# Performance work log

Hardware: AMD Instinct MI355X
Metric: run time of the kernel (lower is better)

## Reference

```python
import jax, jax.numpy as jnp
import numpy as np

I3 = jnp.eye(3, dtype=jnp.float32)
G_VEC = jnp.array([0.0, 0.0, -9.80665], dtype=jnp.float32)
# Q diag: [cov_omega x3, cov_acc x3, cov_b_omega x3, cov_b_acc x3, cov_Rot_c_i x3, cov_t_c_i x3]
Q_DIAG = jnp.array([1e-3] * 3 + [1e-2] * 3 + [6e-9] * 3 + [2e-4] * 3 + [1e-9] * 3 + [1e-9] * 3, dtype=jnp.float32)
N_NORM_ROT = 100
N_NORM_ROT_CI = 1000


def skew(v):
    z = jnp.zeros_like(v[0])
    return jnp.stack([jnp.stack([z, -v[2], v[1]]),
                      jnp.stack([v[2], z, -v[0]]),
                      jnp.stack([-v[1], v[0], z])])


def so3exp(phi):
    a2 = jnp.sum(phi * phi)
    small = a2 < 1e-12
    a = jnp.sqrt(jnp.where(small, 1.0, a2))
    axis = phi / a
    c, s = jnp.cos(a), jnp.sin(a)
    big = c * I3 + (1.0 - c) * jnp.outer(axis, axis) + s * skew(axis)
    return jnp.where(small, I3 + skew(phi), big)


def sen3exp(xi):
    # SE_2(3) exponential: xi[:3]=rotation, xi[3:9]=(v, p) parts
    phi = xi[:3]
    a2 = jnp.sum(phi * phi)
    small = a2 < 1e-12
    a = jnp.sqrt(jnp.where(small, 1.0, a2))
    axis = phi / a
    c, s = jnp.cos(a), jnp.sin(a)
    sk = skew(axis)
    R = jnp.where(small, I3 + skew(phi),
                  c * I3 + (1.0 - c) * jnp.outer(axis, axis) + s * sk)
    J = jnp.where(small, I3 + 0.5 * skew(phi),
                  (s / a) * I3 + (1.0 - s / a) * jnp.outer(axis, axis) + ((1.0 - c) / a) * sk)
    x = J @ xi[3:].reshape(2, 3).T  # (3,2): columns are dv, dp
    return R, x


def normalize_rot(R):
    # Polar-factor re-orthonormalization (equivalent to the SVD-based
    # normalize_rot for near-rotation matrices), via Newton-Schulz iteration
    # which is smooth and jit/vjp friendly.
    def body(X, _):
        return 1.5 * X - 0.5 * (X @ X.T @ X), None
    X, _ = jax.lax.scan(body, R, None, length=8)
    return X


def from_rpy(roll, pitch, yaw):
    cr, sr = jnp.cos(roll), jnp.sin(roll)
    cp, sp = jnp.cos(pitch), jnp.sin(pitch)
    cy, sy = jnp.cos(yaw), jnp.sin(yaw)
    one = jnp.ones_like(cr)
    zero = jnp.zeros_like(cr)
    Rx = jnp.stack([jnp.stack([one, zero, zero]), jnp.stack([zero, cr, -sr]), jnp.stack([zero, sr, cr])])
    Ry = jnp.stack([jnp.stack([cp, zero, sp]), jnp.stack([zero, one, zero]), jnp.stack([-sp, zero, cp])])
    Rz = jnp.stack([jnp.stack([cy, -sy, zero]), jnp.stack([sy, cy, zero]), jnp.stack([zero, zero, one])])
    return Rz @ Ry @ Rx


def init_covariance():
    P = jnp.zeros((21, 21), dtype=jnp.float32)
    P = P.at[:2, :2].set(1e-3 * jnp.eye(2))     # cov_Rot0 (no yaw error)
    P = P.at[3:5, 3:5].set(0.1 * jnp.eye(2))    # cov_v0
    P = P.at[9:12, 9:12].set(6e-3 * I3)         # cov_b_omega0
    P = P.at[12:15, 12:15].set(4e-3 * I3)       # cov_b_acc0
    P = P.at[15:18, 15:18].set(1e-6 * I3)       # cov_Rot_c_i0
    P = P.at[18:21, 18:21].set(5e-3 * I3)       # cov_t_c_i0
    return P


def propagate_cov(P, Rot, v, p, dt):
    F = jnp.zeros((21, 21), dtype=P.dtype)
    F = F.at[3:6, :3].set(skew(G_VEC))
    F = F.at[6:9, 3:6].set(I3)
    F = F.at[:3, 9:12].set(-Rot)
    F = F.at[3:6, 9:12].set(-skew(v) @ Rot)
    F = F.at[3:6, 12:15].set(-Rot)
    F = F.at[6:9, 9:12].set(-skew(p) @ Rot)
    G = jnp.zeros((21, 18), dtype=P.dtype)
    G = G.at[:3, :3].set(Rot)
    G = G.at[3:6, 3:6].set(Rot)
    G = G.at[9:12, 6:9].set(I3)
    G = G.at[12:15, 9:12].set(I3)
    G = G.at[15:18, 12:15].set(I3)
    G = G.at[18:21, 15:18].set(I3)
    F = F * dt
    G = G * dt
    F2 = F @ F
    Phi = jnp.eye(21, dtype=P.dtype) + F + 0.5 * F2 + (F2 @ F) / 6.0  # 3rd-order expm
    return Phi @ (P + (G * Q_DIAG[None, :]) @ G.T) @ Phi.T


def _step(carry, xs):
    Rot, v, p, b_om, b_ac, Rci, tci, P = carry
    u_i, dt_i, mcov_i, i = xs
    # ---- propagate ----
    acc = Rot @ (u_i[3:6] - b_ac) + G_VEC
    v_n = v + acc * dt_i
    p_n = p + v * dt_i + 0.5 * acc * dt_i * dt_i
    Rot_n = Rot @ so3exp((u_i[:3] - b_om) * dt_i)
    P_n = propagate_cov(P, Rot, v, p, dt_i)
    # ---- update: zero lateral/vertical body-velocity pseudo-measurement ----
    omega = u_i[:3] - b_om
    Rot_body = Rot_n @ Rci
    v_imu = Rot_n.T @ v_n
    v_body = Rci.T @ v_imu + skew(tci) @ omega
    H = jnp.zeros((2, 21), dtype=P.dtype)
    H = H.at[:, 3:6].set(Rot_body.T[1:])
    H = H.at[:, 15:18].set((Rci.T @ skew(v_imu))[1:])
    H = H.at[:, 9:12].set(skew(tci)[1:])
    H = H.at[:, 18:21].set(-skew(omega)[1:])
    r = -v_body[1:]
    Rm = jnp.diag(mcov_i)
    S = H @ P_n @ H.T + Rm                    # (2,2)
    K = jnp.linalg.solve(S, H @ P_n).T        # K = P H^T S^-1 (P, S symmetric)
    dx = K @ r                                 # (21,)
    dR, dxi = sen3exp(dx[:9])
    Rot_u = dR @ Rot_n
    v_u = dR @ v_n + dxi[:, 0]
    p_u = dR @ p_n + dxi[:, 1]
    b_om_u = b_om + dx[9:12]
    b_ac_u = b_ac + dx[12:15]
    Rci_u = so3exp(dx[15:18]) @ Rci
    tci_u = tci + dx[18:21]
    IKH = jnp.eye(21, dtype=P.dtype) - K @ H
    P_u = IKH @ P_n @ IKH.T + K @ Rm @ K.T    # Joseph form
    P_u = 0.5 * (P_u + P_u.T)
    Rot_u = jnp.where(i % N_NORM_ROT == 0, normalize_rot(Rot_u), Rot_u)
    Rci_u = jnp.where(i % N_NORM_ROT_CI == 0, normalize_rot(Rci_u), Rci_u)
    carry = (Rot_u, v_u, p_u, b_om_u, b_ac_u, Rci_u, tci_u, P_u)
    return carry, (Rot_u, v_u, p_u, b_om_u, b_ac_u, Rci_u, tci_u)


def _forward(t, u, measurements_covs, v_mes, p_mes, ang0, N):
    dt = t[1:N] - t[:N - 1]
    Rot0 = from_rpy(ang0[0], ang0[1], ang0[2])
    z3 = jnp.zeros(3, dtype=u.dtype)
    carry0 = (Rot0, v_mes[0], z3, z3, z3, I3, z3, init_covariance())
    xs = (u[1:N], dt, measurements_covs[1:N], jnp.arange(1, N))
    _, ys = jax.lax.scan(_step, carry0, xs)
    Rot = jnp.concatenate([Rot0[None], ys[0]], axis=0)
    v = jnp.concatenate([v_mes[0][None], ys[1]], axis=0)
    p = jnp.concatenate([z3[None], ys[2]], axis=0)
    b_omega = jnp.concatenate([z3[None], ys[3]], axis=0)
    b_acc = jnp.concatenate([z3[None], ys[4]], axis=0)
    Rot_c_i = jnp.concatenate([I3[None], ys[5]], axis=0)
    t_c_i = jnp.concatenate([z3[None], ys[6]], axis=0)
    return (Rot, v, p, b_omega, b_acc, Rot_c_i, t_c_i)


def setup_inputs() -> dict:
    key = jax.random.key(0)
    N = 20000  # 200 s at 100 Hz IMU
    k0, k1, k2, k3, k4, k5 = jax.random.split(key, 6)
    t = jnp.arange(N, dtype=jnp.float32) * 0.01
    gyro = 0.01 * jax.random.normal(k0, (N, 3), dtype=jnp.float32)
    acc = jnp.array([0.0, 0.0, 9.80665], jnp.float32) + 0.1 * jax.random.normal(k1, (N, 3), dtype=jnp.float32)
    u = jnp.concatenate([gyro, acc], axis=1)
    measurements_covs = 0.1 + jax.random.uniform(k2, (N, 2), dtype=jnp.float32)
    v_mes = jax.random.normal(k3, (N, 3), dtype=jnp.float32)
    p_mes = jax.random.normal(k4, (N, 3), dtype=jnp.float32)
    ang0 = 0.01 * jax.random.normal(k5, (3,), dtype=jnp.float32)
    return dict(t=t, u=u, measurements_covs=measurements_covs, v_mes=v_mes, p_mes=p_mes, ang0=ang0, N=N)


def reference(t, u, measurements_covs, v_mes, p_mes, ang0, N):
    return _forward(t, u, measurements_covs, v_mes, p_mes, ang0, N)
```

## Files before the change

### kernel.cpp

```cpp
#include <hip/hip_runtime.h>

#define GRAV 9.80665f
#define WAVE_SYNC() do { \
    asm volatile("s_waitcnt lgkmcnt(0)" ::: "memory"); \
    __builtin_amdgcn_sched_barrier(0); \
  } while(0)

#define LDP 28

__device__ __forceinline__ float sel3(int r, float a0, float a1, float a2){
  float x = (r==1)? a1 : a0;
  return (r>=2)? a2 : x;
}
__device__ __forceinline__ float RL(float v, int k){
  return __int_as_float(__builtin_amdgcn_readlane(__float_as_int(v), k));
}
__device__ __forceinline__ float pick9(int k, const float* X){
  float s=X[0];
  s=(k==1)?X[1]:s; s=(k==2)?X[2]:s; s=(k==3)?X[3]:s; s=(k==4)?X[4]:s;
  s=(k==5)?X[5]:s; s=(k==6)?X[6]:s; s=(k==7)?X[7]:s; s=(k==8)?X[8]:s;
  return s;
}

__device__ __forceinline__ void mm33(float* __restrict__ O, const float* A, const float* B){
#pragma unroll
  for(int r=0;r<3;++r){
#pragma unroll
    for(int c=0;c<3;++c){
      O[r*3+c] = A[r*3+0]*B[0*3+c] + A[r*3+1]*B[1*3+c] + A[r*3+2]*B[2*3+c];
    }
  }
}

__device__ __forceinline__ void rot_from_t2(float t_, float p0, float p1, float p2, float* R){
  float c_, k1_, k2_;
  if (t_ < 1e-4f){
    c_  = 1.f - t_*(0.5f - t_*((1.f/24.f) - t_*(1.f/720.f)));
    k2_ = 1.f - t_*((1.f/6.f) - t_*((1.f/120.f) - t_*(1.f/5040.f)));
    k1_ = 0.5f - t_*((1.f/24.f) - t_*(1.f/720.f));
  } else {
    float a = sqrtf(t_);
    c_ = __cosf(a);
    float s = __sinf(a);
    k2_ = s/a;
    k1_ = (1.f - c_)/t_;
  }
  R[0]=c_+k1_*p0*p0;      R[1]=k1_*p0*p1-k2_*p2;  R[2]=k1_*p0*p2+k2_*p1;
  R[3]=k1_*p0*p1+k2_*p2;  R[4]=c_+k1_*p1*p1;      R[5]=k1_*p1*p2-k2_*p0;
  R[6]=k1_*p0*p2-k2_*p1;  R[7]=k1_*p1*p2+k2_*p0;  R[8]=c_+k1_*p2*p2;
}

__device__ __forceinline__ void normalize_rot9(float* X){
#pragma unroll 1
  for(int it=0; it<8; ++it){
    float Y[9], Z[9];
#pragma unroll
    for(int r=0;r<3;++r)
#pragma unroll
      for(int c=0;c<3;++c)
        Y[r*3+c] = X[r*3+0]*X[c*3+0] + X[r*3+1]*X[c*3+1] + X[r*3+2]*X[c*3+2];
#pragma unroll
    for(int r=0;r<3;++r)
#pragma unroll
      for(int c=0;c<3;++c)
        Z[r*3+c] = Y[r*3+0]*X[0*3+c] + Y[r*3+1]*X[1*3+c] + Y[r*3+2]*X[2*3+c];
#pragma unroll
    for(int e=0;e<9;++e) X[e] = 1.5f*X[e] - 0.5f*Z[e];
  }
}

__device__ __forceinline__ float pick_state(int l,
    const float* Rt, const float* vv, const float* pp,
    const float* bw, const float* ba, const float* Rc, const float* tc){
  float s = Rt[0];
  s=(l==1)?Rt[1]:s;  s=(l==2)?Rt[2]:s;  s=(l==3)?Rt[3]:s;  s=(l==4)?Rt[4]:s;
  s=(l==5)?Rt[5]:s;  s=(l==6)?Rt[6]:s;  s=(l==7)?Rt[7]:s;  s=(l==8)?Rt[8]:s;
  s=(l==9)?vv[0]:s;  s=(l==10)?vv[1]:s; s=(l==11)?vv[2]:s;
  s=(l==12)?pp[0]:s; s=(l==13)?pp[1]:s; s=(l==14)?pp[2]:s;
  s=(l==15)?bw[0]:s; s=(l==16)?bw[1]:s; s=(l==17)?bw[2]:s;
  s=(l==18)?ba[0]:s; s=(l==19)?ba[1]:s; s=(l==20)?ba[2]:s;
  s=(l==21)?Rc[0]:s; s=(l==22)?Rc[1]:s; s=(l==23)?Rc[2]:s;
  s=(l==24)?Rc[3]:s; s=(l==25)?Rc[4]:s; s=(l==26)?Rc[5]:s;
  s=(l==27)?Rc[6]:s; s=(l==28)?Rc[7]:s; s=(l==29)?Rc[8]:s;
  s=(l==30)?tc[0]:s; s=(l==31)?tc[1]:s; s=(l==32)?tc[2]:s;
  return s;
}

__global__ __launch_bounds__(64,1)
void iekf_scan_kernel(const float* __restrict__ t,
                      const float* __restrict__ u,
                      const float* __restrict__ mcov,
                      const float* __restrict__ v_mes,
                      const float* __restrict__ ang0,
                      float* __restrict__ out, int N)
{
  const int l = threadIdx.x;
  __shared__ __align__(16) float Pm[21*LDP];
  __shared__ __align__(16) float Eb[21*LDP];

  for (int e=l; e<21*LDP; e+=64){
    int r=e/LDP, c=e-(e/LDP)*LDP;
    float vI=0.f;
    if (r==c){
      if (r<2) vI=0.001f;
      else if (r==3||r==4) vI=0.1f;
      else if (r>=9&&r<12) vI=0.006f;
      else if (r>=12&&r<15) vI=0.004f;
      else if (r>=15&&r<18) vI=1e-6f;
      else if (r>=18&&r<21) vI=0.005f;
    }
    Pm[e]=vI;
  }

  int ostr=0; float* op = out;
  {
    int obase=0, ooff=0;
    if (l<9)       {obase=0;    ostr=9; ooff=l;}
    else if (l<12) {obase=9*N;  ostr=3; ooff=l-9;}
    else if (l<15) {obase=12*N; ostr=3; ooff=l-12;}
    else if (l<18) {obase=15*N; ostr=3; ooff=l-15;}
    else if (l<21) {obase=18*N; ostr=3; ooff=l-18;}
    else if (l<30) {obase=21*N; ostr=9; ooff=l-21;}
    else           {obase=30*N; ostr=3; ooff=l-30;}
    op = out + obase + ooff;
  }

  const int g21 = l/21;
  const int c21 = l - g21*21;
  const int cw  = 9 + 4*g21;
  int l1 = l+21; if (l1>=63) l1-=63;
  int l2 = l+42; if (l2>=63) l2-=63;
  static const int cols[12] = {3,4,5, 9,10,11, 15,16,17, 18,19,20};

  float myval = 0.f;
  {
    float Rt0[9], vv0[3], pp0[3], bwa[3], baa[3], Rc0[9], tca[3];
    float rl = ang0[0], pt = ang0[1], yw = ang0[2];
    float cr=cosf(rl), sr=sinf(rl), cp=cosf(pt), sp=sinf(pt), cy=cosf(yw), sy=sinf(yw);
    Rt0[0]=cy*cp; Rt0[1]=cy*sp*sr - sy*cr; Rt0[2]=cy*sp*cr + sy*sr;
    Rt0[3]=sy*cp; Rt0[4]=sy*sp*sr + cy*cr; Rt0[5]=sy*sp*cr - cy*sr;
    Rt0[6]=-sp;   Rt0[7]=cp*sr;            Rt0[8]=cp*cr;
    vv0[0]=v_mes[0]; vv0[1]=v_mes[1]; vv0[2]=v_mes[2];
#pragma unroll
    for(int k=0;k<3;++k){ pp0[k]=0.f; bwa[k]=0.f; baa[k]=0.f; tca[k]=0.f; }
    Rc0[0]=1.f;Rc0[1]=0.f;Rc0[2]=0.f;Rc0[3]=0.f;Rc0[4]=1.f;Rc0[5]=0.f;Rc0[6]=0.f;Rc0[7]=0.f;Rc0[8]=1.f;
    float sv = pick_state(l, Rt0, vv0, pp0, bwa, baa, Rc0, tca);
    if (l<33){ op[0] = sv; myval = sv; }
  }
  WAVE_SYNC();

  float tA = t[0], tB = t[1];
  float cu[6];
#pragma unroll
  for(int k=0;k<6;++k) cu[k]=u[6+k];
  float cm0=mcov[2], cm1=mcov[3];

  int nx100=100, nx1000=1000;

#pragma unroll 1
  for (int i=1; i<N; ++i){
    float dt = tB - tA;
    float u0=cu[0], u1=cu[1], u2=cu[2], u3=cu[3], u4=cu[4], u5=cu[5];
    float crm0=cm0, crm1=cm1;
    if (i+1 < N){
      tA = tB; tB = t[i+1];
#pragma unroll
      for(int k=0;k<6;++k) cu[k]=u[(i+1)*6+k];
      cm0 = mcov[(i+1)*2]; cm1 = mcov[(i+1)*2+1];
    }

    float Rt[9];
#pragma unroll
    for(int k=0;k<9;++k) Rt[k] = RL(myval, k);
    float vv0s=RL(myval,9),  vv1s=RL(myval,10), vv2s=RL(myval,11);
    float pp0s=RL(myval,12), pp1s=RL(myval,13), pp2s=RL(myval,14);
    float bw0=RL(myval,15),  bw1=RL(myval,16),  bw2=RL(myval,17);
    float ba0=RL(myval,18),  ba1=RL(myval,19),  ba2=RL(myval,20);
    float Rc[9];
#pragma unroll
    for(int k=0;k<9;++k) Rc[k] = RL(myval, 21+k);
    float tc0=RL(myval,30), tc1=RL(myval,31), tc2=RL(myval,32);

    float dt2=dt*dt, gdt=GRAV*dt, hdt=0.5f*dt, hdt2=0.5f*dt*dt;
    float hgdt2 = 0.5f*gdt*dt;
    float g6d   = gdt*dt2*(1.0f/6.0f);

    float w0=u0-bw0, w1=u1-bw1, w2=u2-bw2;
    float aa0=u3-ba0, aa1=u4-ba1, aa2=u5-ba2;
    float acc0 = Rt[0]*aa0+Rt[1]*aa1+Rt[2]*aa2;
    float acc1 = Rt[3]*aa0+Rt[4]*aa1+Rt[5]*aa2;
    float acc2 = Rt[6]*aa0+Rt[7]*aa1+Rt[8]*aa2 - GRAV;
    float vn0=vv0s+acc0*dt, vn1=vv1s+acc1*dt, vn2=vv2s+acc2*dt;
    float pn0=pp0s+vv0s*dt+acc0*hdt2;
    float pn1=pp1s+vv1s*dt+acc1*hdt2;
    float pn2=pp2s+vv2s*dt+acc2*hdt2;
    float ph0=w0*dt, ph1=w1*dt, ph2=w2*dt;
    float dRs[9]; rot_from_t2(ph0*ph0+ph1*ph1+ph2*ph2, ph0,ph1,ph2, dRs);
    float Rn[9]; mm33(Rn, Rt, dRs);

    float RtG[3], RtA[3], RtB[3];
#pragma unroll
    for(int k=0;k<3;++k){
      float r0=Rt[k], r3=Rt[3+k], r6=Rt[6+k];
      RtG[k] = sel3(g21, r0, r3, r6);
      RtA[k] = sel3(g21, r3, r6, r0);
      RtB[k] = sel3(g21, r6, r0, r3);
    }
    float vAs = sel3(g21, vv2s, vv0s, vv1s), vBs = sel3(g21, vv1s, vv2s, vv0s);
    float pAs = sel3(g21, pp2s, pp0s, pp1s), pBs = sel3(g21, pp1s, pp2s, pp0s);
    float Bs0,Bs1,Bs2, Cs0,Cs1,Cs2, Ds0,Ds1,Ds2;
    {
      float bs[3], cs[3], ds[3];
#pragma unroll
      for(int k=0;k<3;++k){
        bs[k] = -dt*RtG[k];
        float craw = dt*(vAs*RtA[k] - vBs*RtB[k]);
        float selC = sel3(g21, -RtA[k], RtB[k], 0.f);
        cs[k] = craw + hgdt2*selC;
        float draw = dt*(pAs*RtA[k] - pBs*RtB[k]);
        ds[k] = draw + hdt*craw + g6d*selC;
      }
      Bs0=bs[0];Bs1=bs[1];Bs2=bs[2];
      Cs0=cs[0];Cs1=cs[1];Cs2=cs[2];
      Ds0=ds[0];Ds1=ds[1];Ds2=ds[2];
    }

    float q0d=0.001f*dt2, q1d=0.01f*dt2;
    float q69=6e-9f*dt2, q24=2e-4f*dt2, q19=1e-9f*dt2;

    if (l<63){
      int c = c21;
      const float4* Pr4 = (const float4*)(Pm + c*LDP);
      float4 a0=Pr4[0], a1=Pr4[1], a2=Pr4[2], a3=Pr4[3], a4=Pr4[4];
      float m20 = Pm[c*LDP + 20];

      bool cl3 = (c<3);
      bool c36 = (c>=3 && c<6);
      int csel = c36 ? (c-3) : (cl3 ? c : 0);
      float Rtc0 = sel3(csel, Rt[0], Rt[3], Rt[6]);
      float Rtc1 = sel3(csel, Rt[1], Rt[4], Rt[7]);
      float Rtc2 = sel3(csel, Rt[2], Rt[5], Rt[8]);
      float dot0 = Rt[0]*Rtc0 + Rt[1]*Rtc1 + Rt[2]*Rtc2;
      float dot1 = Rt[3]*Rtc0 + Rt[4]*Rtc1 + Rt[5]*Rtc2;
      float dotg = RtG[0]*Rtc0 + RtG[1]*Rtc1 + RtG[2]*Rtc2;

      float m0  = a0.x + (cl3 ? q0d*dot0 : 0.f);
      float m1  = a0.y + (cl3 ? q0d*dot1 : 0.f);
      float mr  = sel3(g21, a0.x, a0.y, a0.z) + (cl3 ? q0d*dotg : 0.f);
      float m3r = sel3(g21, a0.w, a1.x, a1.y) + (c36 ? q1d*dotg : 0.f);
      float m6r = sel3(g21, a1.z, a1.w, a2.x);
      float m9  = a2.y + ((c==9) ? q69 : 0.f);
      float m10 = a2.z + ((c==10)? q69 : 0.f);
      float m11 = a2.w + ((c==11)? q69 : 0.f);
      float m12 = a3.x + ((c==12)? q24 : 0.f);
      float m13 = a3.y + ((c==13)? q24 : 0.f);
      float m14 = a3.z + ((c==14)? q24 : 0.f);

      float Ar = (g21==0)? gdt*m1 : (g21==1)? -gdt*m0 : 0.f;
      float bterm = Bs0*m12+Bs1*m13+Bs2*m14;
      float e0 = mr + Bs0*m9+Bs1*m10+Bs2*m11;
      float e1 = m3r + Ar + Cs0*m9+Cs1*m10+Cs2*m11 + bterm;
      float e2 = m6r + hdt*Ar + dt*m3r + Ds0*m9+Ds1*m10+Ds2*m11 + hdt*bterm;
      Eb[g21*LDP+c]=e0; Eb[(3+g21)*LDP+c]=e1; Eb[(6+g21)*LDP+c]=e2;

      float mc0 = sel3(g21, a2.y, a3.y, a4.y);
      float mc1 = sel3(g21, a2.z, a3.z, a4.z);
      float mc2 = sel3(g21, a2.w, a3.w, a4.w);
      float mc3 = sel3(g21, a3.x, a4.x, m20);
      float qd0 = sel3(g21, q69, q24, q19);
      float qd1 = sel3(g21, q69, q24, q19);
      float qd2 = sel3(g21, q69, q19, q19);
      float qd3 = sel3(g21, q24, q19, q19);
      Eb[(cw+0)*LDP+c] = mc0 + ((cw+0==c)? qd0 : 0.f);
      Eb[(cw+1)*LDP+c] = mc1 + ((cw+1==c)? qd1 : 0.f);
      Eb[(cw+2)*LDP+c] = mc2 + ((cw+2==c)? qd2 : 0.f);
      Eb[(cw+3)*LDP+c] = mc3 + ((cw+3==c)? qd3 : 0.f);
    }

    float H0[12], H1[12];
    float rr0, rr1;
    {
      float Rb1 = Rn[0]*Rc[1]+Rn[1]*Rc[4]+Rn[2]*Rc[7];
      float Rb4 = Rn[3]*Rc[1]+Rn[4]*Rc[4]+Rn[5]*Rc[7];
      float Rb7 = Rn[6]*Rc[1]+Rn[7]*Rc[4]+Rn[8]*Rc[7];
      float Rb2 = Rn[0]*Rc[2]+Rn[1]*Rc[5]+Rn[2]*Rc[8];
      float Rb5 = Rn[3]*Rc[2]+Rn[4]*Rc[5]+Rn[5]*Rc[8];
      float Rb8 = Rn[6]*Rc[2]+Rn[7]*Rc[5]+Rn[8]*Rc[8];
      float vi0 = Rn[0]*vn0+Rn[3]*vn1+Rn[6]*vn2;
      float vi1 = Rn[1]*vn0+Rn[4]*vn1+Rn[7]*vn2;
      float vi2 = Rn[2]*vn0+Rn[5]*vn1+Rn[8]*vn2;
      float vb1 = Rc[1]*vi0+Rc[4]*vi1+Rc[7]*vi2 + (tc2*w0 - tc0*w2);
      float vb2 = Rc[2]*vi0+Rc[5]*vi1+Rc[8]*vi2 + (tc0*w1 - tc1*w0);
      rr0 = -vb1; rr1 = -vb2;
      H0[0]=Rb1; H0[1]=Rb4; H0[2]=Rb7;
      H1[0]=Rb2; H1[1]=Rb5; H1[2]=Rb8;
      H0[3]=tc2;  H0[4]=0.f;  H0[5]=-tc0;
      H1[3]=-tc1; H1[4]=tc0;  H1[5]=0.f;
      H0[6]=Rc[4]*vi2 - Rc[7]*vi1;  H0[7]=Rc[7]*vi0 - Rc[1]*vi2;  H0[8]=Rc[1]*vi1 - Rc[4]*vi0;
      H1[6]=Rc[5]*vi2 - Rc[8]*vi1;  H1[7]=Rc[8]*vi0 - Rc[2]*vi2;  H1[8]=Rc[2]*vi1 - Rc[5]*vi0;
      H0[9]=-w2; H0[10]=0.f; H0[11]=w0;
      H1[9]=w1;  H1[10]=-w0; H1[11]=0.f;
    }
    WAVE_SYNC();

    float pnv[7];
#pragma unroll
    for(int k=0;k<7;++k) pnv[k]=0.f;
    float p0=0.f, p1=0.f;
    if (l<63){
      int r = c21;
      const float4* Er4 = (const float4*)(Eb + r*LDP);
      float4 a0=Er4[0], a1=Er4[1], a2=Er4[2], a3=Er4[3], a4=Er4[4];
      float e20 = Eb[r*LDP + 20];

      float e0a=a0.x, e1a=a0.y;
      float eg  = sel3(g21, a0.x, a0.y, a0.z);
      float e3g = sel3(g21, a0.w, a1.x, a1.y);
      float e6g = sel3(g21, a1.z, a1.w, a2.x);
      float e9=a2.y, e10=a2.z, e11=a2.w, e12=a3.x, e13=a3.y, e14=a3.z;

      float Ag = (g21==0)? gdt*e1a : (g21==1)? -gdt*e0a : 0.f;
      float bterm = Bs0*e12+Bs1*e13+Bs2*e14;
      pnv[0] = eg + Bs0*e9+Bs1*e10+Bs2*e11;
      pnv[1] = e3g + Ag + Cs0*e9+Cs1*e10+Cs2*e11 + bterm;
      pnv[2] = e6g + hdt*Ag + dt*e3g + Ds0*e9+Ds1*e10+Ds2*e11 + hdt*bterm;
      pnv[3] = sel3(g21, a2.y, a3.y, a4.y);
      pnv[4] = sel3(g21, a2.z, a3.z, a4.z);
      pnv[5] = sel3(g21, a2.w, a3.w, a4.w);
      pnv[6] = sel3(g21, a3.x, a4.x, e20);

      float c1a = sel3(g21, H0[0], H0[1], H0[2]);
      float c3a = sel3(g21, H0[3], 0.f,   H0[8]);
      float c4a = sel3(g21, H0[4], 0.f,   H0[9]);
      float c5a = sel3(g21, H0[5], H0[6], H0[10]);
      float c6a = sel3(g21, 0.f,   H0[7], H0[11]);
      float c1b = sel3(g21, H1[0], H1[1], H1[2]);
      float c3b = sel3(g21, H1[3], 0.f,   H1[8]);
      float c4b = sel3(g21, H1[4], 0.f,   H1[9]);
      float c5b = sel3(g21, H1[5], H1[6], H1[10]);
      float c6b = sel3(g21, 0.f,   H1[7], H1[11]);
      p0 = c1a*pnv[1] + c3a*pnv[3] + c4a*pnv[4] + c5a*pnv[5] + c6a*pnv[6];
      p1 = c1b*pnv[1] + c3b*pnv[3] + c4b*pnv[4] + c5b*pnv[5] + c6b*pnv[6];
    }
    float hpr0 = p0 + __shfl(p0, l1) + __shfl(p0, l2);
    float hpr1 = p1 + __shfl(p1, l1) + __shfl(p1, l2);

    float hpjx[7], hpjy[7];
#pragma unroll
    for (int s=0;s<7;++s){
      int j = (s<3)? (g21 + 3*s) : (cw + (s-3));
      hpjx[s] = __shfl(hpr0, j);
      hpjy[s] = __shfl(hpr1, j);
    }

    float hph00=0.f, hph01=0.f, hph10=0.f, hph11=0.f;
#pragma unroll
    for(int k=0;k<12;++k){
      float hp0 = RL(hpr0, cols[k]);
      float hp1 = RL(hpr1, cols[k]);
      hph00 += hp0*H0[k]; hph01 += hp0*H1[k];
      hph10 += hp1*H0[k]; hph11 += hp1*H1[k];
    }
    float s00 = hph00 + crm0, s01 = hph01, s10 = hph10, s11 = hph11 + crm1;
    float idet = 1.0f/(s00*s11 - s01*s10);
    float i00 =  s11*idet, i01 = -s01*idet, i10 = -s10*idet, i11 = s00*idet;
    float K0 = i00*hpr0 + i01*hpr1;
    float K1 = i10*hpr0 + i11*hpr1;
    float s01q = 0.5f*(s01 + s10);
    float dxval = K0*rr0 + K1*rr1;

    float dx0 = RL(dxval,0), dx1 = RL(dxval,1), dx2 = RL(dxval,2);
    float dx3 = RL(dxval,3), dx4 = RL(dxval,4), dx5 = RL(dxval,5);
    float dx6 = RL(dxval,6), dx7 = RL(dxval,7), dx8 = RL(dxval,8);
    float dx15 = RL(dxval,15), dx16 = RL(dxval,16), dx17 = RL(dxval,17);
    int src = (l>=30 && l<33)? (l-12) : ((l>=15 && l<21)? (l-6) : 0);
    float dxadd = __shfl(dxval, src);

    if (l<63){
      int r = c21;
#pragma unroll
      for (int s=0;s<7;++s){
        int j = (s<3)? (g21 + 3*s) : (cw + (s-3));
        float kjx = i00*hpjx[s] + i01*hpjy[s];
        float kjy = i10*hpjx[s] + i11*hpjy[s];
        float cross = (K0*hpjx[s] + K1*hpjy[s]) + (kjx*hpr0 + kjy*hpr1);
        float quad  = (K0*kjx)*s00 + (K0*kjy + K1*kjx)*s01q + (K1*kjy)*s11;
        float val = pnv[s] - cross + quad;
        if (r <= j){
          Pm[r*LDP+j] = val;
          if (r < j) Pm[j*LDP+r] = val;
        }
      }
    }

    float t2x = dx0*dx0+dx1*dx1+dx2*dx2;
    float cX,k1X,k2X,j1X;
    if (t2x < 1e-4f){
      cX  = 1.f - t2x*(0.5f - t2x*((1.f/24.f) - t2x*(1.f/720.f)));
      k2X = 1.f - t2x*((1.f/6.f) - t2x*((1.f/120.f) - t2x*(1.f/5040.f)));
      k1X = 0.5f - t2x*((1.f/24.f) - t2x*(1.f/720.f));
      j1X = (1.f/6.f) - t2x*((1.f/120.f) - t2x*(1.f/5040.f));
    } else {
      float a = sqrtf(t2x);
      cX = __cosf(a);
      float s = __sinf(a);
      k2X = s/a; k1X = (1.f-cX)/t2x; j1X = (1.f-k2X)/t2x;
    }
    float dR[9];
    dR[0]=cX+k1X*dx0*dx0;      dR[1]=k1X*dx0*dx1-k2X*dx2; dR[2]=k1X*dx0*dx2+k2X*dx1;
    dR[3]=k1X*dx0*dx1+k2X*dx2; dR[4]=cX+k1X*dx1*dx1;      dR[5]=k1X*dx1*dx2-k2X*dx0;
    dR[6]=k1X*dx0*dx2-k2X*dx1; dR[7]=k1X*dx1*dx2+k2X*dx0; dR[8]=cX+k1X*dx2*dx2;
    float Jm[9];
    Jm[0]=k2X+j1X*dx0*dx0;      Jm[1]=j1X*dx0*dx1-k1X*dx2; Jm[2]=j1X*dx0*dx2+k1X*dx1;
    Jm[3]=j1X*dx0*dx1+k1X*dx2;  Jm[4]=k2X+j1X*dx1*dx1;     Jm[5]=j1X*dx1*dx2-k1X*dx0;
    Jm[6]=j1X*dx0*dx2-k1X*dx1;  Jm[7]=j1X*dx1*dx2+k1X*dx0; Jm[8]=k2X+j1X*dx2*dx2;
    float Ec[9];
    rot_from_t2(dx15*dx15+dx16*dx16+dx17*dx17, dx15,dx16,dx17, Ec);

    float nv = 0.f;
    if (l<9){
      int ro=(l>=6)?2:((l>=3)?1:0); int co=l-3*ro;
      float d0=sel3(ro,dR[0],dR[3],dR[6]), d1=sel3(ro,dR[1],dR[4],dR[7]), d2=sel3(ro,dR[2],dR[5],dR[8]);
      float n0=sel3(co,Rn[0],Rn[1],Rn[2]), n1=sel3(co,Rn[3],Rn[4],Rn[5]), n2=sel3(co,Rn[6],Rn[7],Rn[8]);
      nv = d0*n0 + d1*n1 + d2*n2;
    } else if (l<15){
      int j=l-9; bool isv=(j<3); int ro = isv? j : (j-3);
      float x0 = isv? vn0:pn0, x1 = isv? vn1:pn1, x2 = isv? vn2:pn2;
      float y0 = isv? dx3:dx6, y1 = isv? dx4:dx7, y2 = isv? dx5:dx8;
      float d0=sel3(ro,dR[0],dR[3],dR[6]), d1=sel3(ro,dR[1],dR[4],dR[7]), d2=sel3(ro,dR[2],dR[5],dR[8]);
      float j0=sel3(ro,Jm[0],Jm[3],Jm[6]), j1m=sel3(ro,Jm[1],Jm[4],Jm[7]), j2m=sel3(ro,Jm[2],Jm[5],Jm[8]);
      nv = d0*x0 + d1*x1 + d2*x2 + j0*y0 + j1m*y1 + j2m*y2;
    } else if (l<21){
      float old = (l<18)? sel3(l-15,bw0,bw1,bw2) : sel3(l-18,ba0,ba1,ba2);
      nv = old + dxadd;
    } else if (l<30){
      int j=l-21; int ro=(j>=6)?2:((j>=3)?1:0); int co=j-3*ro;
      float e0=sel3(ro,Ec[0],Ec[3],Ec[6]), e1=sel3(ro,Ec[1],Ec[4],Ec[7]), e2=sel3(ro,Ec[2],Ec[5],Ec[8]);
      float r0=sel3(co,Rc[0],Rc[1],Rc[2]), r1=sel3(co,Rc[3],Rc[4],Rc[5]), r2=sel3(co,Rc[6],Rc[7],Rc[8]);
      nv = e0*r0 + e1*r1 + e2*r2;
    } else if (l<33){
      nv = sel3(l-30,tc0,tc1,tc2) + dxadd;
    }
    if (l<33) myval = nv;

    bool n100 = (i==nx100), n1000 = (i==nx1000);
    if (n100) nx100 += 100;
    if (n1000) nx1000 += 1000;
    if (n100 || n1000){
      if (n100){
        float X[9];
#pragma unroll
        for (int k=0;k<9;++k) X[k]=RL(myval,k);
        normalize_rot9(X);
        if (l<9) myval = pick9(l,X);
      }
      if (n1000){
        float Y[9];
#pragma unroll
        for (int k=0;k<9;++k) Y[k]=RL(myval,21+k);
        normalize_rot9(Y);
        if (l>=21 && l<30) myval = pick9(l-21,Y);
      }
    }

    if (l<33) op[i*ostr] = myval;

    WAVE_SYNC();
  }
}

extern "C" void kernel_launch(void* const* d_in, const int* in_sizes, int n_in,
                              void* d_out, int out_size, void* d_ws, size_t ws_size,
                              hipStream_t stream) {
  (void)n_in; (void)out_size; (void)d_ws; (void)ws_size;
  const float* t     = (const float*)d_in[0];
  const float* u     = (const float*)d_in[1];
  const float* mcov  = (const float*)d_in[2];
  const float* v_mes = (const float*)d_in[3];
  const float* ang0  = (const float*)d_in[5];
  int N = in_sizes[0];
  iekf_scan_kernel<<<dim3(1), dim3(64), 0, stream>>>(t, u, mcov, v_mes, ang0, (float*)d_out, N);
}
```

Measured before the change: 49.86 ms.

## Stage HP and K through LDS, symmetrize P update, hoist propagation block

Replaces the 14 per-lane shuffles that gathered HP columns with LDS staging of HP and K vectors. The covariance update now writes every entry, using the average of the mirrored predicted entries read from a new transposed LDS buffer, instead of conditional symmetric writes. The update is moved after the dR/Jm and Ec computation, with a wave sync in between. The propagation block is also hoisted earlier so its LDS writes can overlap the state computation. This adds LDS traffic and a wait on the critical path of the serial scan.

```diff
diff --git a/kernel.cpp b/kernel.cpp
--- a/kernel.cpp
+++ b/kernel.cpp
@@ -97,6 +97,9 @@
   const int l = threadIdx.x;
   __shared__ __align__(16) float Pm[21*LDP];
   __shared__ __align__(16) float Eb[21*LDP];
+  __shared__ __align__(16) float PnS[21*LDP];
+  __shared__ float2 HPs2[21];
+  __shared__ float2 Ks2[21];
 
   for (int e=l; e<21*LDP; e+=64){
     int r=e/LDP, c=e-(e/LDP)*LDP;
@@ -184,6 +187,85 @@
     float dt2=dt*dt, gdt=GRAV*dt, hdt=0.5f*dt, hdt2=0.5f*dt*dt;
     float hgdt2 = 0.5f*gdt*dt;
     float g6d   = gdt*dt2*(1.0f/6.0f);
+
+    float RtG[3], RtA[3], RtB[3];
+#pragma unroll
+    for(int k=0;k<3;++k){
+      float r0=Rt[k], r3=Rt[3+k], r6=Rt[6+k];
+      RtG[k] = sel3(g21, r0, r3, r6);
+      RtA[k] = sel3(g21, r3, r6, r0);
+      RtB[k] = sel3(g21, r6, r0, r3);
+    }
+    float vAs = sel3(g21, vv2s, vv0s, vv1s), vBs = sel3(g21, vv1s, vv2s, vv0s);
+    float pAs = sel3(g21, pp2s, pp0s, pp1s), pBs = sel3(g21, pp1s, pp2s, pp0s);
+    float Bs0,Bs1,Bs2, Cs0,Cs1,Cs2, Ds0,Ds1,Ds2;
+    {
+      float bs[3], cs[3], ds[3];
+#pragma unroll
+      for(int k=0;k<3;++k){
+        bs[k] = -dt*RtG[k];
+        float craw = dt*(vAs*RtA[k] - vBs*RtB[k]);
+        float selC = sel3(g21, -RtA[k], RtB[k], 0.f);
+        cs[k] = craw + hgdt2*selC;
+        float draw = dt*(pAs*RtA[k] - pBs*RtB[k]);
+        ds[k] = draw + hdt*craw + g6d*selC;
+      }
+      Bs0=bs[0];Bs1=bs[1];Bs2=bs[2];
+      Cs0=cs[0];Cs1=cs[1];Cs2=cs[2];
+      Ds0=ds[0];Ds1=ds[1];Ds2=ds[2];
+    }
+
+    float q0d=0.001f*dt2, q1d=0.01f*dt2;
+    float q69=6e-9f*dt2, q24=2e-4f*dt2, q19=1e-9f*dt2;
+
+    if (l<63){
+      int c = c21;
+      const float4* Pr4 = (const float4*)(Pm + c*LDP);
+      float4 a0=Pr4[0], a1=Pr4[1], a2=Pr4[2], a3=Pr4[3], a4=Pr4[4];
+      float m20 = Pm[c*LDP + 20];
+
+      bool cl3 = (c<3);
+      bool c36 = (c>=3 && c<6);
+      int csel = c36 ? (c-3) : (cl3 ? c : 0);
+      float Rtc0 = sel3(csel, Rt[0], Rt[3], Rt[6]);
+      float Rtc1 = sel3(csel, Rt[1], Rt[4], Rt[7]);
+      float Rtc2 = sel3(csel, Rt[2], Rt[5], Rt[8]);
+      float dot0 = Rt[0]*Rtc0 + Rt[1]*Rtc1 + Rt[2]*Rtc2;
+      float dot1 = Rt[3]*Rtc0 + Rt[4]*Rtc1 + Rt[5]*Rtc2;
+      float dotg = RtG[0]*Rtc0 + RtG[1]*Rtc1 + RtG[2]*Rtc2;
+
+      float m0  = a0.x + (cl3 ? q0d*dot0 : 0.f);
+      float m1  = a0.y + (cl3 ? q0d*dot1 : 0.f);
+      float mr  = sel3(g21, a0.x, a0.y, a0.z) + (cl3 ? q0d*dotg : 0.f);
+      float m3r = sel3(g21, a0.w, a1.x, a1.y) + (c36 ? q1d*dotg : 0.f);
+      float m6r = sel3(g21, a1.z, a1.w, a2.x);
+      float m9  = a2.y + ((c==9) ? q69 : 0.f);
+      float m10 = a2.z + ((c==10)? q69 : 0.f);
+      float m11 = a2.w + ((c==11)? q69 : 0.f);
+      float m12 = a3.x + ((c==12)? q24 : 0.f);
+      float m13 = a3.y + ((c==13)? q24 : 0.f);
+      float m14 = a3.z + ((c==14)? q24 : 0.f);
+
+      float Ar = (g21==0)? gdt*m1 : (g21==1)? -gdt*m0 : 0.f;
+      float bterm = Bs0*m12+Bs1*m13+Bs2*m14;
+      float e0 = mr + Bs0*m9+Bs1*m10+Bs2*m11;
+      float e1 = m3r + Ar + Cs0*m9+Cs1*m10+Cs2*m11 + bterm;
+      float e2 = m6r + hdt*Ar + dt*m3r + Ds0*m9+Ds1*m10+Ds2*m11 + hdt*bterm;
+      Eb[g21*LDP+c]=e0; Eb[(3+g21)*LDP+c]=e1; Eb[(6+g21)*LDP+c]=e2;
+
+      float mc0 = sel3(g21, a2.y, a3.y, a4.y);
+      float mc1 = sel3(g21, a2.z, a3.z, a4.z);
+      float mc2 = sel3(g21, a2.w, a3.w, a4.w);
+      float mc3 = sel3(g21, a3.x, a4.x, m20);
+      float qd0 = sel3(g21, q69, q24, q19);
+      float qd1 = sel3(g21, q69, q24, q19);
+      float qd2 = sel3(g21, q69, q19, q19);
+      float qd3 = sel3(g21, q24, q19, q19);
+      Eb[(cw+0)*LDP+c] = mc0 + ((cw+0==c)? qd0 : 0.f);
+      Eb[(cw+1)*LDP+c] = mc1 + ((cw+1==c)? qd1 : 0.f);
+      Eb[(cw+2)*LDP+c] = mc2 + ((cw+2==c)? qd2 : 0.f);
+      Eb[(cw+3)*LDP+c] = mc3 + ((cw+3==c)? qd3 : 0.f);
+    }
 
     float w0=u0-bw0, w1=u1-bw1, w2=u2-bw2;
     float aa0=u3-ba0, aa1=u4-ba1, aa2=u5-ba2;
@@ -197,85 +279,6 @@
     float ph0=w0*dt, ph1=w1*dt, ph2=w2*dt;
     float dRs[9]; rot_from_t2(ph0*ph0+ph1*ph1+ph2*ph2, ph0,ph1,ph2, dRs);
     float Rn[9]; mm33(Rn, Rt, dRs);
-
-    float RtG[3], RtA[3], RtB[3];
-#pragma unroll
-    for(int k=0;k<3;++k){
-      float r0=Rt[k], r3=Rt[3+k], r6=Rt[6+k];
-      RtG[k] = sel3(g21, r0, r3, r6);
-      RtA[k] = sel3(g21, r3, r6, r0);
-      RtB[k] = sel3(g21, r6, r0, r3);
-    }
-    float vAs = sel3(g21, vv2s, vv0s, vv1s), vBs = sel3(g21, vv1s, vv2s, vv0s);
-    float pAs = sel3(g21, pp2s, pp0s, pp1s), pBs = sel3(g21, pp1s, pp2s, pp0s);
-    float Bs0,Bs1,Bs2, Cs0,Cs1,Cs2, Ds0,Ds1,Ds2;
-    {
-      float bs[3], cs[3], ds[3];
-#pragma unroll
-      for(int k=0;k<3;++k){
-        bs[k] = -dt*RtG[k];
-        float craw = dt*(vAs*RtA[k] - vBs*RtB[k]);
-        float selC = sel3(g21, -RtA[k], RtB[k], 0.f);
-        cs[k] = craw + hgdt2*selC;
-        float draw = dt*(pAs*RtA[k] - pBs*RtB[k]);
-        ds[k] = draw + hdt*craw + g6d*selC;
-      }
-      Bs0=bs[0];Bs1=bs[1];Bs2=bs[2];
-      Cs0=cs[0];Cs1=cs[1];Cs2=cs[2];
-      Ds0=ds[0];Ds1=ds[1];Ds2=ds[2];
-    }
-
-    float q0d=0.001f*dt2, q1d=0.01f*dt2;
-    float q69=6e-9f*dt2, q24=2e-4f*dt2, q19=1e-9f*dt2;
-
-    if (l<63){
-      int c = c21;
-      const float4* Pr4 = (const float4*)(Pm + c*LDP);
-      float4 a0=Pr4[0], a1=Pr4[1], a2=Pr4[2], a3=Pr4[3], a4=Pr4[4];
-      float m20 = Pm[c*LDP + 20];
-
-      bool cl3 = (c<3);
-      bool c36 = (c>=3 && c<6);
-      int csel = c36 ? (c-3) : (cl3 ? c : 0);
-      float Rtc0 = sel3(csel, Rt[0], Rt[3], Rt[6]);
-      float Rtc1 = sel3(csel, Rt[1], Rt[4], Rt[7]);
-      float Rtc2 = sel3(csel, Rt[2], Rt[5], Rt[8]);
-      float dot0 = Rt[0]*Rtc0 + Rt[1]*Rtc1 + Rt[2]*Rtc2;
-      float dot1 = Rt[3]*Rtc0 + Rt[4]*Rtc1 + Rt[5]*Rtc2;
-      float dotg = RtG[0]*Rtc0 + RtG[1]*Rtc1 + RtG[2]*Rtc2;
-
-      float m0  = a0.x + (cl3 ? q0d*dot0 : 0.f);
-      float m1  = a0.y + (cl3 ? q0d*dot1 : 0.f);
-      float mr  = sel3(g21, a0.x, a0.y, a0.z) + (cl3 ? q0d*dotg : 0.f);
-      float m3r = sel3(g21, a0.w, a1.x, a1.y) + (c36 ? q1d*dotg : 0.f);
-      float m6r = sel3(g21, a1.z, a1.w, a2.x);
-      float m9  = a2.y + ((c==9) ? q69 : 0.f);
-      float m10 = a2.z + ((c==10)? q69 : 0.f);
-      float m11 = a2.w + ((c==11)? q69 : 0.f);
-      float m12 = a3.x + ((c==12)? q24 : 0.f);
-      float m13 = a3.y + ((c==13)? q24 : 0.f);
-      float m14 = a3.z + ((c==14)? q24 : 0.f);
-
-      float Ar = (g21==0)? gdt*m1 : (g21==1)? -gdt*m0 : 0.f;
-      float bterm = Bs0*m12+Bs1*m13+Bs2*m14;
-      float e0 = mr + Bs0*m9+Bs1*m10+Bs2*m11;
-      float e1 = m3r + Ar + Cs0*m9+Cs1*m10+Cs2*m11 + bterm;
-      float e2 = m6r + hdt*Ar + dt*m3r + Ds0*m9+Ds1*m10+Ds2*m11 + hdt*bterm;
-      Eb[g21*LDP+c]=e0; Eb[(3+g21)*LDP+c]=e1; Eb[(6+g21)*LDP+c]=e2;
-
-      float mc0 = sel3(g21, a2.y, a3.y, a4.y);
-      float mc1 = sel3(g21, a2.z, a3.z, a4.z);
-      float mc2 = sel3(g21, a2.w, a3.w, a4.w);
-      float mc3 = sel3(g21, a3.x, a4.x, m20);
-      float qd0 = sel3(g21, q69, q24, q19);
-      float qd1 = sel3(g21, q69, q24, q19);
-      float qd2 = sel3(g21, q69, q19, q19);
-      float qd3 = sel3(g21, q24, q19, q19);
-      Eb[(cw+0)*LDP+c] = mc0 + ((cw+0==c)? qd0 : 0.f);
-      Eb[(cw+1)*LDP+c] = mc1 + ((cw+1==c)? qd1 : 0.f);
-      Eb[(cw+2)*LDP+c] = mc2 + ((cw+2==c)? qd2 : 0.f);
-      Eb[(cw+3)*LDP+c] = mc3 + ((cw+3==c)? qd3 : 0.f);
-    }
 
     float H0[12], H1[12];
     float rr0, rr1;
@@ -329,6 +332,14 @@
       pnv[5] = sel3(g21, a2.w, a3.w, a4.w);
       pnv[6] = sel3(g21, a3.x, a4.x, e20);
 
+      PnS[r*LDP + g21]   = pnv[0];
+      PnS[r*LDP + 3+g21] = pnv[1];
+      PnS[r*LDP + 6+g21] = pnv[2];
+      PnS[r*LDP + cw]    = pnv[3];
+      PnS[r*LDP + cw+1]  = pnv[4];
+      PnS[r*LDP + cw+2]  = pnv[5];
+      PnS[r*LDP + cw+3]  = pnv[6];
+
       float c1a = sel3(g21, H0[0], H0[1], H0[2]);
       float c3a = sel3(g21, H0[3], 0.f,   H0[8]);
       float c4a = sel3(g21, H0[4], 0.f,   H0[9]);
@@ -344,14 +355,7 @@
     }
     float hpr0 = p0 + __shfl(p0, l1) + __shfl(p0, l2);
     float hpr1 = p1 + __shfl(p1, l1) + __shfl(p1, l2);
-
-    float hpjx[7], hpjy[7];
-#pragma unroll
-    for (int s=0;s<7;++s){
-      int j = (s<3)? (g21 + 3*s) : (cw + (s-3));
-      hpjx[s] = __shfl(hpr0, j);
-      hpjy[s] = __shfl(hpr1, j);
-    }
+    if (l<21) HPs2[l] = make_float2(hpr0, hpr1);
 
     float hph00=0.f, hph01=0.f, hph10=0.f, hph11=0.f;
 #pragma unroll
@@ -368,6 +372,7 @@
     float K1 = i10*hpr0 + i11*hpr1;
     float s01q = 0.5f*(s01 + s10);
     float dxval = K0*rr0 + K1*rr1;
+    if (l<21) Ks2[l] = make_float2(K0,K1);
 
     float dx0 = RL(dxval,0), dx1 = RL(dxval,1), dx2 = RL(dxval,2);
     float dx3 = RL(dxval,3), dx4 = RL(dxval,4), dx5 = RL(dxval,5);
@@ -375,23 +380,6 @@
     float dx15 = RL(dxval,15), dx16 = RL(dxval,16), dx17 = RL(dxval,17);
     int src = (l>=30 && l<33)? (l-12) : ((l>=15 && l<21)? (l-6) : 0);
     float dxadd = __shfl(dxval, src);
-
-    if (l<63){
-      int r = c21;
-#pragma unroll
-      for (int s=0;s<7;++s){
-        int j = (s<3)? (g21 + 3*s) : (cw + (s-3));
-        float kjx = i00*hpjx[s] + i01*hpjy[s];
-        float kjy = i10*hpjx[s] + i11*hpjy[s];
-        float cross = (K0*hpjx[s] + K1*hpjy[s]) + (kjx*hpr0 + kjy*hpr1);
-        float quad  = (K0*kjx)*s00 + (K0*kjy + K1*kjx)*s01q + (K1*kjy)*s11;
-        float val = pnv[s] - cross + quad;
-        if (r <= j){
-          Pm[r*LDP+j] = val;
-          if (r < j) Pm[j*LDP+r] = val;
-        }
-      }
-    }
 
     float t2x = dx0*dx0+dx1*dx1+dx2*dx2;
     float cX,k1X,k2X,j1X;
@@ -416,6 +404,23 @@
     Jm[6]=j1X*dx0*dx2-k1X*dx1;  Jm[7]=j1X*dx1*dx2+k1X*dx0; Jm[8]=k2X+j1X*dx2*dx2;
     float Ec[9];
     rot_from_t2(dx15*dx15+dx16*dx16+dx17*dx17, dx15,dx16,dx17, Ec);
+
+    WAVE_SYNC();
+
+    if (l<63){
+      int r = c21;
+#pragma unroll
+      for (int s=0;s<7;++s){
+        int j = (s<3)? (g21 + 3*s) : (cw + (s-3));
+        float pnT = PnS[j*LDP + r];
+        float2 hpj = HPs2[j];
+        float2 kj  = Ks2[j];
+        float base  = 0.5f*(pnv[s] + pnT);
+        float cross = (K0*hpj.x + K1*hpj.y) + (kj.x*hpr0 + kj.y*hpr1);
+        float quad  = (K0*kj.x)*s00 + (K0*kj.y + K1*kj.x)*s01q + (K1*kj.y)*s11;
+        Pm[r*LDP+j] = base - cross + quad;
+      }
+    }
 
     float nv = 0.f;
     if (l<9){
```

Result: no change. 49.68 ms (-0.4%).
